# Optimization experiments

Measured on AMD Instinct MI355X. Metric: run time of the kernel, lower is better.

Reference implementation:

```python
import jax, jax.numpy as jnp
import numpy as np

N = 50000      # nodes
E = 800000     # edges (avg degree 16)
IN = 128       # in_channels
OUT = 64       # out_channels
K = 2          # propagation hops


def setup_inputs() -> dict:
    key = jax.random.key(0)
    k1, k2, k3 = jax.random.split(key, 3)
    x = jax.random.normal(k1, (N, IN), dtype=jnp.float32)
    edge_index = jax.random.randint(k2, (2, E), 0, N, dtype=jnp.int32)
    # SGConv's internal Linear(in, out): weight [OUT, IN], bias [OUT]
    W = jax.random.normal(k3, (OUT, IN), dtype=jnp.float32) / np.sqrt(IN)
    b = jnp.zeros((OUT,), dtype=jnp.float32)
    return {"x": x, "edge_index": edge_index, "W": W, "b": b}


def reference(x, edge_index, W, b):
    # GCN normalization with self-loops (PyG gcn_norm, add_self_loops=True)
    row, col = edge_index[0], edge_index[1]
    loops = jnp.arange(N, dtype=edge_index.dtype)
    row = jnp.concatenate([row, loops])   # source nodes
    col = jnp.concatenate([col, loops])   # target nodes
    ones = jnp.ones((E + N,), dtype=x.dtype)
    deg = jax.ops.segment_sum(ones, col, num_segments=N)          # in-degree incl. self-loop
    deg_inv_sqrt = jnp.where(deg > 0, jax.lax.rsqrt(deg), 0.0)
    norm = deg_inv_sqrt[row] * deg_inv_sqrt[col]                  # [E+N]

    # K-hop propagation: x <- D^{-1/2} (A+I) D^{-1/2} x
    for _ in range(K):
        x = jax.ops.segment_sum(x[row] * norm[:, None], col, num_segments=N)

    # final linear; dropout is identity in eval mode (training=False)
    return x @ W.T + b
```

## Files before the change

kernel.cpp:

```cpp
#include <hip/hip_runtime.h>
#include <hip/hip_bf16.h>
#include <hip/hip_fp16.h>

#define IN_CH 128
#define OUT_CH 64
#define NB 240

__global__ void __launch_bounds__(256) histo_kernel(const int* __restrict__ col,
                                                    int* __restrict__ blkcnt,
                                                    int* __restrict__ totals,
                                                    int E, int chunk) {
    __shared__ int h[256];
    int blk = blockIdx.x, tid = threadIdx.x;
    h[tid] = 0;
    __syncthreads();
    int s = blk * chunk, e = min(s + chunk, E);
    for (int i = s + tid; i < e; i += 256)
        atomicAdd(&h[col[i] >> 8], 1);
    __syncthreads();
    int v = h[tid];
    blkcnt[blk * 256 + tid] = v;
    if (v) atomicAdd(&totals[tid], v);
}

__global__ void __launch_bounds__(256) scan2_kernel(int* __restrict__ blkcnt,
                                                    const int* __restrict__ totals,
                                                    int* __restrict__ bstart,
                                                    int* __restrict__ off,
                                                    int nb, int nbkt, int E, int n) {
    __shared__ int ps[256];
    int tid = threadIdx.x;
    if (blockIdx.x < (unsigned)nbkt) {
        int b = blockIdx.x;
        int v = (tid < nb) ? blkcnt[tid * 256 + b] : 0;
        ps[tid] = v;
        __syncthreads();
        for (int d = 1; d < 256; d <<= 1) {
            int t = 0;
            if (tid >= d) t = ps[tid - d];
            __syncthreads();
            if (tid >= d) ps[tid] += t;
            __syncthreads();
        }
        if (tid < nb) blkcnt[tid * 256 + b] = ps[tid] - v;
    } else {
        int v = (tid < nbkt) ? totals[tid] : 0;
        ps[tid] = v;
        __syncthreads();
        for (int d = 1; d < 256; d <<= 1) {
            int t = 0;
            if (tid >= d) t = ps[tid - d];
            __syncthreads();
            if (tid >= d) ps[tid] += t;
            __syncthreads();
        }
        if (tid < nbkt) bstart[tid] = ps[tid] - v;
        if (tid == 0) { bstart[nbkt] = E; off[n] = E; }
    }
}

__global__ void __launch_bounds__(256) bucket_scatter_kernel(const int* __restrict__ row,
                                                             const int* __restrict__ col,
                                                             const int* __restrict__ blkcnt,
                                                             const int* __restrict__ bstart,
                                                             unsigned int* __restrict__ tmp,
                                                             int E, int chunk, int nbkt) {
    __shared__ int cur[256];
    int blk = blockIdx.x, tid = threadIdx.x;
    cur[tid] = (tid < nbkt) ? bstart[tid] + blkcnt[blk * 256 + tid] : 0;
    __syncthreads();
    int s = blk * chunk, e = min(s + chunk, E);
    for (int i = s + tid; i < e; i += 256) {
        int c = col[i], r = row[i];
        int p = atomicAdd(&cur[c >> 8], 1);
        tmp[p] = ((unsigned)(c & 255) << 16) | (unsigned)r;
    }
}

__global__ void __launch_bounds__(256) bucket_sort_kernel(const unsigned int* __restrict__ tmp,
                                                          const int* __restrict__ bstart,
                                                          int* __restrict__ off,
                                                          float* __restrict__ dis,
                                                          unsigned short* __restrict__ eidx,
                                                          int n) {
    __shared__ int cntl[256];
    __shared__ int sc[256];
    __shared__ int posl[256];
    int b = blockIdx.x, tid = threadIdx.x;
    int s = bstart[b], e = bstart[b + 1];
    cntl[tid] = 0;
    __syncthreads();
    for (int i = s + tid; i < e; i += 256)
        atomicAdd(&cntl[tmp[i] >> 16], 1);
    __syncthreads();
    int c = cntl[tid];
    sc[tid] = c;
    __syncthreads();
    for (int d = 1; d < 256; d <<= 1) {
        int t = 0;
        if (tid >= d) t = sc[tid - d];
        __syncthreads();
        if (tid >= d) sc[tid] += t;
        __syncthreads();
    }
    int excl = sc[tid] - c;
    int gid = (b << 8) + tid;
    if (gid < n) {
        off[gid] = s + excl;
        dis[gid] = rsqrtf((float)(c + 1));
    }
    posl[tid] = s + excl;
    __syncthreads();
    for (int i = s + tid; i < e; i += 256) {
        unsigned int v = tmp[i];
        int p = atomicAdd(&posl[v >> 16], 1);
        eidx[p] = (unsigned short)(v & 0xFFFFu);
    }
}

__global__ void __launch_bounds__(256, 2) gemm_kernel(const float* __restrict__ x,
                                                      const float* __restrict__ W,
                                                      const float* __restrict__ dis,
                                                      __half* __restrict__ z, int n) {
    __shared__ float Xs[64 * 132];
    __shared__ float Ws[64 * 132];
    int t = threadIdx.x;
    int m0 = blockIdx.x * 64;
#pragma unroll
    for (int r = 0; r < 8; ++r) {
        int f = t + 256 * r;
        int o = f >> 5, kq = f & 31;
        float4 w = ((const float4*)W)[f];
        *(float4*)&Ws[o * 132 + kq * 4] = w;
    }
#pragma unroll
    for (int r = 0; r < 8; ++r) {
        int f = t + 256 * r;
        int node = f >> 5, kq = f & 31;
        int gv = min(m0 + node, n - 1);
        float4 xv = ((const float4*)(x + (size_t)gv * IN_CH))[kq];
        *(float4*)&Xs[node * 132 + kq * 4] = xv;
    }
    __syncthreads();
    int tx = t & 15, ty = t >> 4;
    float acc[4][4];
#pragma unroll
    for (int i = 0; i < 4; ++i)
#pragma unroll
        for (int j = 0; j < 4; ++j) acc[i][j] = 0.f;

#pragma unroll 4
    for (int kq = 0; kq < 32; ++kq) {
        float4 xa[4], wb[4];
#pragma unroll
        for (int i = 0; i < 4; ++i) xa[i] = *(const float4*)&Xs[(tx + 16 * i) * 132 + kq * 4];
#pragma unroll
        for (int j = 0; j < 4; ++j) wb[j] = *(const float4*)&Ws[(ty * 4 + j) * 132 + kq * 4];
#pragma unroll
        for (int i = 0; i < 4; ++i)
#pragma unroll
            for (int j = 0; j < 4; ++j) {
                float s = acc[i][j];
                s = fmaf(xa[i].x, wb[j].x, s);
                s = fmaf(xa[i].y, wb[j].y, s);
                s = fmaf(xa[i].z, wb[j].z, s);
                s = fmaf(xa[i].w, wb[j].w, s);
                acc[i][j] = s;
            }
    }
#pragma unroll
    for (int i = 0; i < 4; ++i) {
        int v = m0 + tx + 16 * i;
        if (v < n) {
            float dv = dis[v];
            union { __half2 h[2]; float2 f; } u;
            u.h[0] = __floats2half2_rn(dv * acc[i][0], dv * acc[i][1]);
            u.h[1] = __floats2half2_rn(dv * acc[i][2], dv * acc[i][3]);
            *(float2*)&z[(size_t)v * OUT_CH + ty * 4] = u.f;
        }
    }
}

template <int MODE>
__global__ void __launch_bounds__(256) hop_kernel(const __half* __restrict__ zin,
                                                  void* __restrict__ out,
                                                  const unsigned short* __restrict__ eidx,
                                                  const int* __restrict__ off,
                                                  const float* __restrict__ dis,
                                                  const float* __restrict__ bias, int n) {
    int v = (int)((blockIdx.x * 256 + threadIdx.x) >> 6);
    if (v >= n) return;
    int lane = threadIdx.x & 63;
    int grp = lane >> 3;
    int sub = lane & 7;
    int s = off[v], e = off[v + 1];
    float a0 = 0.f, a1 = 0.f, a2 = 0.f, a3 = 0.f;
    float a4 = 0.f, a5 = 0.f, a6 = 0.f, a7 = 0.f;
    if (grp == 0) {
        float4 raw = ((const float4*)(zin + (size_t)v * OUT_CH))[sub];
        const __half2* h2 = (const __half2*)&raw;
        float2 f0 = __half22float2(h2[0]), f1 = __half22float2(h2[1]);
        float2 f2 = __half22float2(h2[2]), f3 = __half22float2(h2[3]);
        a0 = f0.x; a1 = f0.y; a2 = f1.x; a3 = f1.y;
        a4 = f2.x; a5 = f2.y; a6 = f3.x; a7 = f3.y;
    }
    int i = s + grp;
    bool have = (i < e);
    int r = have ? (int)eidx[i] : 0;
    while (have) {
        int j = i + 8;
        bool hnext = (j < e);
        int rn = hnext ? (int)eidx[j] : 0;
        float4 raw = ((const float4*)(zin + (size_t)r * OUT_CH))[sub];
        const __half2* h2 = (const __half2*)&raw;
        float2 f0 = __half22float2(h2[0]), f1 = __half22float2(h2[1]);
        float2 f2 = __half22float2(h2[2]), f3 = __half22float2(h2[3]);
        a0 += f0.x; a1 += f0.y; a2 += f1.x; a3 += f1.y;
        a4 += f2.x; a5 += f2.y; a6 += f3.x; a7 += f3.y;
        r = rn; i = j; have = hnext;
    }
#pragma unroll
    for (int m = 8; m <= 32; m <<= 1) {
        a0 += __shfl_xor(a0, m, 64); a1 += __shfl_xor(a1, m, 64);
        a2 += __shfl_xor(a2, m, 64); a3 += __shfl_xor(a3, m, 64);
        a4 += __shfl_xor(a4, m, 64); a5 += __shfl_xor(a5, m, 64);
        a6 += __shfl_xor(a6, m, 64); a7 += __shfl_xor(a7, m, 64);
    }
    if (grp == 0) {
        float dv = dis[v];
        if (MODE == 0) {
            float sc = dv * dv;
            union { __half2 h[4]; float4 f; } u;
            u.h[0] = __floats2half2_rn(sc * a0, sc * a1);
            u.h[1] = __floats2half2_rn(sc * a2, sc * a3);
            u.h[2] = __floats2half2_rn(sc * a4, sc * a5);
            u.h[3] = __floats2half2_rn(sc * a6, sc * a7);
            ((float4*)((__half*)out + (size_t)v * OUT_CH))[sub] = u.f;
        } else {
            const float4* bp = (const float4*)(bias + sub * 8);
            float4 b0 = bp[0], b1 = bp[1];
            float* op = (float*)out + (size_t)v * OUT_CH + sub * 8;
            *(float4*)op = make_float4(fmaf(dv, a0, b0.x), fmaf(dv, a1, b0.y),
                                       fmaf(dv, a2, b0.z), fmaf(dv, a3, b0.w));
            *(float4*)(op + 4) = make_float4(fmaf(dv, a4, b1.x), fmaf(dv, a5, b1.y),
                                             fmaf(dv, a6, b1.z), fmaf(dv, a7, b1.w));
        }
    }
}

extern "C" void kernel_launch(void* const* d_in, const int* in_sizes, int n_in,
                              void* d_out, int out_size, void* d_ws, size_t ws_size,
                              hipStream_t stream) {
    const float* x = (const float*)d_in[0];
    const int* ei = (const int*)d_in[1];
    const float* W = (const float*)d_in[2];
    const float* b = (const float*)d_in[3];
    int n = in_sizes[0] / IN_CH;
    int E = in_sizes[1] / 2;
    const int* row = ei;
    const int* col = ei + E;

    char* ws = (char*)d_ws;
    size_t o = 0;
    auto alloc = [&](size_t bytes) -> void* {
        void* p = ws + o;
        o += (bytes + 255) & ~(size_t)255;
        return p;
    };
    int nbkt = (n + 255) >> 8;
    int chunk = (E + NB - 1) / NB;

    int*            blkcnt = (int*)alloc((size_t)NB * 256 * 4);
    int*            totals = (int*)alloc(256 * 4);
    int*            bstart = (int*)alloc((size_t)(nbkt + 1) * 4);
    unsigned int*   tmp    = (unsigned int*)alloc((size_t)E * 4);
    int*            off    = (int*)alloc((size_t)(n + 1) * 4);
    float*          dis    = (float*)alloc((size_t)n * 4);
    unsigned short* eidx   = (unsigned short*)alloc((size_t)E * 2);
    __half*         zA     = (__half*)alloc((size_t)n * OUT_CH * 2);
    __half*         zB     = (__half*)alloc((size_t)n * OUT_CH * 2);

    hipMemsetAsync(totals, 0, 256 * 4, stream);
    histo_kernel<<<NB, 256, 0, stream>>>(col, blkcnt, totals, E, chunk);
    scan2_kernel<<<nbkt + 1, 256, 0, stream>>>(blkcnt, totals, bstart, off, NB, nbkt, E, n);
    bucket_scatter_kernel<<<NB, 256, 0, stream>>>(row, col, blkcnt, bstart, tmp, E, chunk, nbkt);
    bucket_sort_kernel<<<nbkt, 256, 0, stream>>>(tmp, bstart, off, dis, eidx, n);
    gemm_kernel<<<(n + 63) / 64, 256, 0, stream>>>(x, W, dis, zA, n);
    int hopBlocks = (n + 3) / 4;
    hop_kernel<0><<<hopBlocks, 256, 0, stream>>>(zA, zB, eidx, off, dis, nullptr, n);
    hop_kernel<1><<<hopBlocks, 256, 0, stream>>>(zB, d_out, eidx, off, dis, b, n);
}
```

Measured before the change: 174.3 us.

## Restructure CSR bucket sort: drop global atomics and memset, widen blocks

The histogram no longer accumulates bucket totals with global atomics, so the memset of the totals buffer goes away. The per-bucket scan now produces the totals, and the scan over bucket starts is recomputed redundantly inside the scatter and sort kernels rather than in a separate block. Block count and threads per block rise to 512 to add parallelism in the histogram, scatter and sort phases. The price is redundant 256-entry scans in every block, plus scanblk assuming exactly 512 histogram blocks.

```diff
diff --git a/kernel.cpp b/kernel.cpp
--- a/kernel.cpp
+++ b/kernel.cpp
@@ -4,117 +4,127 @@
 
 #define IN_CH 128
 #define OUT_CH 64
-#define NB 240
-
-__global__ void __launch_bounds__(256) histo_kernel(const int* __restrict__ col,
+#define NB 512
+
+__global__ void __launch_bounds__(512) histo_kernel(const int* __restrict__ col,
                                                     int* __restrict__ blkcnt,
-                                                    int* __restrict__ totals,
                                                     int E, int chunk) {
     __shared__ int h[256];
     int blk = blockIdx.x, tid = threadIdx.x;
-    h[tid] = 0;
+    if (tid < 256) h[tid] = 0;
     __syncthreads();
     int s = blk * chunk, e = min(s + chunk, E);
-    for (int i = s + tid; i < e; i += 256)
+    for (int i = s + tid; i < e; i += 512)
         atomicAdd(&h[col[i] >> 8], 1);
     __syncthreads();
-    int v = h[tid];
-    blkcnt[blk * 256 + tid] = v;
-    if (v) atomicAdd(&totals[tid], v);
-}
-
-__global__ void __launch_bounds__(256) scan2_kernel(int* __restrict__ blkcnt,
-                                                    const int* __restrict__ totals,
-                                                    int* __restrict__ bstart,
-                                                    int* __restrict__ off,
-                                                    int nb, int nbkt, int E, int n) {
+    if (tid < 256) blkcnt[blk * 256 + tid] = h[tid];
+}
+
+__global__ void __launch_bounds__(256) scanblk_kernel(int* __restrict__ blkcnt,
+                                                      int* __restrict__ totals) {
     __shared__ int ps[256];
-    int tid = threadIdx.x;
-    if (blockIdx.x < (unsigned)nbkt) {
-        int b = blockIdx.x;
-        int v = (tid < nb) ? blkcnt[tid * 256 + b] : 0;
-        ps[tid] = v;
-        __syncthreads();
-        for (int d = 1; d < 256; d <<= 1) {
-            int t = 0;
-            if (tid >= d) t = ps[tid - d];
-            __syncthreads();
-            if (tid >= d) ps[tid] += t;
-            __syncthreads();
-        }
-        if (tid < nb) blkcnt[tid * 256 + b] = ps[tid] - v;
-    } else {
-        int v = (tid < nbkt) ? totals[tid] : 0;
-        ps[tid] = v;
-        __syncthreads();
-        for (int d = 1; d < 256; d <<= 1) {
-            int t = 0;
-            if (tid >= d) t = ps[tid - d];
-            __syncthreads();
-            if (tid >= d) ps[tid] += t;
-            __syncthreads();
-        }
-        if (tid < nbkt) bstart[tid] = ps[tid] - v;
-        if (tid == 0) { bstart[nbkt] = E; off[n] = E; }
-    }
-}
-
-__global__ void __launch_bounds__(256) bucket_scatter_kernel(const int* __restrict__ row,
+    int b = blockIdx.x, tid = threadIdx.x;
+    int i0 = (2 * tid) * 256 + b, i1 = (2 * tid + 1) * 256 + b;
+    int a0 = blkcnt[i0], a1 = blkcnt[i1];
+    int lsum = a0 + a1;
+    ps[tid] = lsum;
+    __syncthreads();
+    for (int d = 1; d < 256; d <<= 1) {
+        int t = 0;
+        if (tid >= d) t = ps[tid - d];
+        __syncthreads();
+        if (tid >= d) ps[tid] += t;
+        __syncthreads();
+    }
+    int excl = ps[tid] - lsum;
+    blkcnt[i0] = excl;
+    blkcnt[i1] = excl + a0;
+    if (tid == 255) totals[b] = excl + lsum;
+}
+
+__global__ void __launch_bounds__(512) bucket_scatter_kernel(const int* __restrict__ row,
                                                              const int* __restrict__ col,
                                                              const int* __restrict__ blkcnt,
-                                                             const int* __restrict__ bstart,
+                                                             const int* __restrict__ totals,
                                                              unsigned int* __restrict__ tmp,
                                                              int E, int chunk, int nbkt) {
+    __shared__ int ps[256];
     __shared__ int cur[256];
     int blk = blockIdx.x, tid = threadIdx.x;
-    cur[tid] = (tid < nbkt) ? bstart[tid] + blkcnt[blk * 256 + tid] : 0;
+    int v = 0;
+    if (tid < 256) { v = (tid < nbkt) ? totals[tid] : 0; ps[tid] = v; }
+    __syncthreads();
+    for (int d = 1; d < 256; d <<= 1) {
+        int t = 0;
+        if (tid < 256 && tid >= d) t = ps[tid - d];
+        __syncthreads();
+        if (tid < 256 && tid >= d) ps[tid] += t;
+        __syncthreads();
+    }
+    if (tid < 256) cur[tid] = (ps[tid] - v) + blkcnt[blk * 256 + tid];
     __syncthreads();
     int s = blk * chunk, e = min(s + chunk, E);
-    for (int i = s + tid; i < e; i += 256) {
+    for (int i = s + tid; i < e; i += 512) {
         int c = col[i], r = row[i];
         int p = atomicAdd(&cur[c >> 8], 1);
         tmp[p] = ((unsigned)(c & 255) << 16) | (unsigned)r;
     }
 }
 
-__global__ void __launch_bounds__(256) bucket_sort_kernel(const unsigned int* __restrict__ tmp,
-                                                          const int* __restrict__ bstart,
+__global__ void __launch_bounds__(512) bucket_sort_kernel(const unsigned int* __restrict__ tmp,
+                                                          const int* __restrict__ totals,
                                                           int* __restrict__ off,
                                                           float* __restrict__ dis,
                                                           unsigned short* __restrict__ eidx,
-                                                          int n) {
+                                                          int nbkt, int E, int n) {
+    __shared__ int bs[256];
     __shared__ int cntl[256];
     __shared__ int sc[256];
     __shared__ int posl[256];
     int b = blockIdx.x, tid = threadIdx.x;
-    int s = bstart[b], e = bstart[b + 1];
-    cntl[tid] = 0;
-    __syncthreads();
-    for (int i = s + tid; i < e; i += 256)
-        atomicAdd(&cntl[tmp[i] >> 16], 1);
-    __syncthreads();
-    int c = cntl[tid];
-    sc[tid] = c;
+    int v = 0;
+    if (tid < 256) { v = (tid < nbkt) ? totals[tid] : 0; bs[tid] = v; }
     __syncthreads();
     for (int d = 1; d < 256; d <<= 1) {
         int t = 0;
-        if (tid >= d) t = sc[tid - d];
-        __syncthreads();
-        if (tid >= d) sc[tid] += t;
-        __syncthreads();
-    }
-    int excl = sc[tid] - c;
-    int gid = (b << 8) + tid;
-    if (gid < n) {
-        off[gid] = s + excl;
-        dis[gid] = rsqrtf((float)(c + 1));
-    }
-    posl[tid] = s + excl;
-    __syncthreads();
-    for (int i = s + tid; i < e; i += 256) {
-        unsigned int v = tmp[i];
-        int p = atomicAdd(&posl[v >> 16], 1);
-        eidx[p] = (unsigned short)(v & 0xFFFFu);
+        if (tid < 256 && tid >= d) t = bs[tid - d];
+        __syncthreads();
+        if (tid < 256 && tid >= d) bs[tid] += t;
+        __syncthreads();
+    }
+    if (tid < 256) bs[tid] -= v;
+    if (tid < 256) cntl[tid] = 0;
+    __syncthreads();
+    int s = bs[b];
+    int e = s + ((b < nbkt) ? totals[b] : 0);
+    for (int i = s + tid; i < e; i += 512)
+        atomicAdd(&cntl[tmp[i] >> 16], 1);
+    __syncthreads();
+    int c = 0, excl = 0;
+    if (tid < 256) { c = cntl[tid]; sc[tid] = c; }
+    __syncthreads();
+    for (int d = 1; d < 256; d <<= 1) {
+        int t = 0;
+        if (tid < 256 && tid >= d) t = sc[tid - d];
+        __syncthreads();
+        if (tid < 256 && tid >= d) sc[tid] += t;
+        __syncthreads();
+    }
+    if (tid < 256) {
+        excl = sc[tid] - c;
+        int gid = (b << 8) + tid;
+        if (gid < n) {
+            off[gid] = s + excl;
+            dis[gid] = rsqrtf((float)(c + 1));
+        }
+        posl[tid] = s + excl;
+    }
+    if (b == 0 && tid == 0) off[n] = E;
+    __syncthreads();
+    for (int i = s + tid; i < e; i += 512) {
+        unsigned int w = tmp[i];
+        int p = atomicAdd(&posl[w >> 16], 1);
+        eidx[p] = (unsigned short)(w & 0xFFFFu);
     }
 }
 
@@ -272,7 +282,6 @@
 
     int*            blkcnt = (int*)alloc((size_t)NB * 256 * 4);
     int*            totals = (int*)alloc(256 * 4);
-    int*            bstart = (int*)alloc((size_t)(nbkt + 1) * 4);
     unsigned int*   tmp    = (unsigned int*)alloc((size_t)E * 4);
     int*            off    = (int*)alloc((size_t)(n + 1) * 4);
     float*          dis    = (float*)alloc((size_t)n * 4);
@@ -280,11 +289,10 @@
     __half*         zA     = (__half*)alloc((size_t)n * OUT_CH * 2);
     __half*         zB     = (__half*)alloc((size_t)n * OUT_CH * 2);
 
-    hipMemsetAsync(totals, 0, 256 * 4, stream);
-    histo_kernel<<<NB, 256, 0, stream>>>(col, blkcnt, totals, E, chunk);
-    scan2_kernel<<<nbkt + 1, 256, 0, stream>>>(blkcnt, totals, bstart, off, NB, nbkt, E, n);
-    bucket_scatter_kernel<<<NB, 256, 0, stream>>>(row, col, blkcnt, bstart, tmp, E, chunk, nbkt);
-    bucket_sort_kernel<<<nbkt, 256, 0, stream>>>(tmp, bstart, off, dis, eidx, n);
+    histo_kernel<<<NB, 512, 0, stream>>>(col, blkcnt, E, chunk);
+    scanblk_kernel<<<nbkt, 256, 0, stream>>>(blkcnt, totals);
+    bucket_scatter_kernel<<<NB, 512, 0, stream>>>(row, col, blkcnt, totals, tmp, E, chunk, nbkt);
+    bucket_sort_kernel<<<nbkt, 512, 0, stream>>>(tmp, totals, off, dis, eidx, nbkt, E, n);
     gemm_kernel<<<(n + 63) / 64, 256, 0, stream>>>(x, W, dis, zA, n);
     int hopBlocks = (n + 3) / 4;
     hop_kernel<0><<<hopBlocks, 256, 0, stream>>>(zA, zB, eidx, off, dis, nullptr, n);
```

Measured after the change: 167.9 us. -3.6%, faster.
